# Kernel tuning notes

Measured on AMD Instinct MI355X. Metric: run time of the kernel, lower is better.

The kernel has to match this reference:

```python
import jax, jax.numpy as jnp
import numpy as np

HEADS = 4


def setup_inputs() -> dict:
    key = jax.random.key(0)
    ks = jax.random.split(key, 6)
    b, c, d, h, w = 4, 512, 16, 16, 16
    x = jax.random.normal(ks[0], (b, c, d, h, w), dtype=jnp.float32)
    s = 0.02  # param init scale
    Wq = jax.random.normal(ks[1], (c, c), dtype=jnp.float32) * s
    Wk = jax.random.normal(ks[2], (c, c), dtype=jnp.float32) * s
    Wv = jax.random.normal(ks[3], (c, c), dtype=jnp.float32) * s
    Wproj = jax.random.normal(ks[4], (c, c), dtype=jnp.float32) * s
    bproj = jnp.zeros((c,), dtype=jnp.float32)
    return {"x": x, "Wq": Wq, "Wk": Wk, "Wv": Wv, "Wproj": Wproj, "bproj": bproj}


def reference(x, Wq, Wk, Wv, Wproj, bproj):
    b, c, d, h, w = x.shape
    N = d * h * w
    scale = (c // HEADS) ** -0.5  # module uses ch//heads for scale
    xf = x.reshape(b, c, N)  # (b, c, N)
    # 1x1 Conv1d == channel matmul
    q = jnp.einsum('oc,bcn->bon', Wq, xf)
    k = jnp.einsum('oc,bcn->bon', Wk, xf)
    v = jnp.einsum('oc,bcn->bon', Wv, xf)
    # Faithful to original (buggy) view: split SEQUENCE dim by heads -> (b, H, c, N//H)
    q = q.reshape(b, HEADS, c, N // HEADS)
    k = k.reshape(b, HEADS, c, N // HEADS)
    v = v.reshape(b, HEADS, c, N // HEADS)
    attn = jax.nn.softmax(jnp.einsum('bhqe,bhke->bhqk', q, k) * scale, axis=-1)
    out = jnp.einsum('bhqk,bhke->bhqe', attn, v)  # (b, H, c, N//H)
    out = jnp.swapaxes(out, 2, 3).reshape(b, c, N)  # matches transpose(2,3).view
    out = jnp.einsum('oc,bcn->bon', Wproj, out) + bproj[None, :, None]
    return out.reshape(b, c, d, h, w) + x
```

## Files before the change

kernel.cpp:

```cpp
#include <hip/hip_runtime.h>
#include <stdint.h>


typedef __attribute__((ext_vector_type(8))) short short8;
typedef __attribute__((ext_vector_type(4))) float f32x4;

typedef const __attribute__((address_space(1))) unsigned int* gas_ptr;
typedef __attribute__((address_space(3))) unsigned int* las_ptr;

#define ATTN_SCALE 0.08838834764831845f

__device__ __forceinline__ unsigned short f2bf(float f) {
    union { float f; unsigned int u; } c; c.f = f;
    unsigned int u = c.u;
    u += 0x7fffu + ((u >> 16) & 1u);
    return (unsigned short)(u >> 16);
}

__device__ __forceinline__ void gl_lds16(const void* g, void* l) {
    __builtin_amdgcn_global_load_lds((gas_ptr)(uintptr_t)g, (las_ptr)(uintptr_t)l,
                                     16, 0, 0);
}

template<int LDA, int LDB, int KDIM, bool PERMB = false>
__device__ __forceinline__ void mfma_core(
    const unsigned short* __restrict__ A,
    const unsigned short* __restrict__ B,
    int m0, int n0,
    unsigned short* __restrict__ sA, unsigned short* __restrict__ sB,
    f32x4 acc[4][4])
{
    const int tid  = threadIdx.x;
    const int lane = tid & 63, wave = tid >> 6;
    const int lr = lane >> 2, lc = lane & 3;
    const int lcs = lc ^ ((lr >> 1) & 3);
    const int wm = (wave & 1) * 64, wn = (wave >> 1) * 64;
    const int col = lane & 15, quad = lane >> 4;
    const int swz = (quad ^ ((col >> 1) & 3)) * 8;

    const unsigned short* ga = A + (size_t)(m0 + 32 * wave + lr) * LDA + lcs * 8;
    int rb0 = n0 + 32 * wave + lr;
    int rb1 = rb0 + 16;
    if (PERMB) {
        rb0 = 4 * (rb0 & 127) + (rb0 >> 7);
        rb1 = 4 * (rb1 & 127) + (rb1 >> 7);
    }
    const unsigned short* gb0 = B + (size_t)rb0 * LDB + lcs * 8;
    const unsigned short* gb1 = B + (size_t)rb1 * LDB + lcs * 8;

    const int wr0 = (32 * wave) * 32;
    const int wr1 = (32 * wave + 16) * 32;

    gl_lds16(ga,            sA + wr0);
    gl_lds16(ga + 16 * LDA, sA + wr1);
    gl_lds16(gb0,           sB + wr0);
    gl_lds16(gb1,           sB + wr1);

    constexpr int NK = KDIM / 32;
    for (int kk = 0; kk < NK; ++kk) {
        const int bo = (kk & 1) * 4096;
        if (kk + 1 < NK) {
            const int nb = ((kk + 1) & 1) * 4096;
            const int k0 = (kk + 1) * 32;
            gl_lds16(ga + k0,            sA + nb + wr0);
            gl_lds16(ga + k0 + 16 * LDA, sA + nb + wr1);
            gl_lds16(gb0 + k0,           sB + nb + wr0);
            gl_lds16(gb1 + k0,           sB + nb + wr1);
            asm volatile("s_waitcnt vmcnt(4)" ::: "memory");
        } else {
            asm volatile("s_waitcnt vmcnt(0)" ::: "memory");
        }
        __builtin_amdgcn_s_barrier();
        asm volatile("" ::: "memory");
        __builtin_amdgcn_sched_barrier(0);

        const unsigned short* bA = sA + bo;
        const unsigned short* bB = sB + bo;
        short8 af[4], bfv[4];
        #pragma unroll
        for (int i = 0; i < 4; ++i)
            af[i] = *(const short8*)&bA[(wm + i * 16 + col) * 32 + swz];
        #pragma unroll
        for (int j = 0; j < 4; ++j)
            bfv[j] = *(const short8*)&bB[(wn + j * 16 + col) * 32 + swz];
        #pragma unroll
        for (int i = 0; i < 4; ++i)
            #pragma unroll
            for (int j = 0; j < 4; ++j)
                acc[i][j] = __builtin_amdgcn_mfma_f32_16x16x32_bf16(
                    af[i], bfv[j], acc[i][j], 0, 0, 0);

        __builtin_amdgcn_s_barrier();
        asm volatile("" ::: "memory");
    }
}

__global__ __launch_bounds__(256)
void prep(const float* __restrict__ x,
          const float* __restrict__ Wq, const float* __restrict__ Wk,
          const float* __restrict__ Wv, const float* __restrict__ Wp,
          unsigned short* __restrict__ xT, unsigned short* __restrict__ Wb)
{
    if (blockIdx.z == 4) {
        const int idx = (blockIdx.y * 64 + blockIdx.x) * 256 + threadIdx.x;
        const int mat = idx >> 16;
        const int off = (idx & 65535) << 2;
        const float* src = (mat == 0 ? Wq : mat == 1 ? Wk : mat == 2 ? Wv : Wp) + off;
        const float4 f = *(const float4*)src;
        uint2 o;
        o.x = f2bf(f.x) | ((unsigned)f2bf(f.y) << 16);
        o.y = f2bf(f.z) | ((unsigned)f2bf(f.w) << 16);
        *(uint2*)&Wb[mat * 262144 + off] = o;
        return;
    }
    const int b = blockIdx.z;
    const int l = threadIdx.x & 63, w = threadIdx.x >> 6;
    const int n  = blockIdx.x * 64 + l;
    const int c0 = blockIdx.y * 32 + w * 8;
    const float* xp = x + (size_t)b * 2097152 + (size_t)c0 * 4096 + n;
    unsigned int p[4];
    #pragma unroll
    for (int j = 0; j < 4; ++j) {
        const unsigned short a  = f2bf(xp[(2 * j)     * 4096]);
        const unsigned short bb = f2bf(xp[(2 * j + 1) * 4096]);
        p[j] = a | ((unsigned)bb << 16);
    }
    uint4 v; v.x = p[0]; v.y = p[1]; v.z = p[2]; v.w = p[3];
    *(uint4*)&xT[(size_t)b * 2097152 + (size_t)n * 512 + c0] = v;
}

__global__ __launch_bounds__(256)
void gemm_qkv(const unsigned short* __restrict__ Wb,
              const unsigned short* __restrict__ xT,
              unsigned short* __restrict__ qb, unsigned short* __restrict__ kb,
              unsigned short* __restrict__ vT)
{
    __shared__ unsigned short sA[2 * 128 * 32], sB[2 * 128 * 32];

    const int z = blockIdx.z, wsel = z >> 2, b = z & 3;
    const unsigned short* A = Wb + wsel * 262144;
    const unsigned short* B = xT + (size_t)b * 2097152;
    const int m0 = blockIdx.y * 128, n0 = blockIdx.x * 128;

    f32x4 z4 = {0.f, 0.f, 0.f, 0.f};
    f32x4 acc[4][4];
    #pragma unroll
    for (int i = 0; i < 4; ++i)
        #pragma unroll
        for (int j = 0; j < 4; ++j) acc[i][j] = z4;

    mfma_core<512, 512, 512>(A, B, m0, n0, sA, sB, acc);

    const int lane = threadIdx.x & 63, wave = threadIdx.x >> 6;
    const int wm = (wave & 1) * 64, wn = (wave >> 1) * 64;
    const int col = lane & 15, quad = lane >> 4;

    if (wsel < 2) {
        unsigned short* C = (wsel == 0 ? qb : kb) + (size_t)b * 2097152;
        #pragma unroll
        for (int i = 0; i < 4; ++i)
            #pragma unroll
            for (int r = 0; r < 4; ++r) {
                const int row = m0 + wm + i * 16 + quad * 4 + r;
                #pragma unroll
                for (int j = 0; j < 4; ++j)
                    C[(size_t)row * 4096 + n0 + wn + j * 16 + col] = f2bf(acc[i][j][r]);
            }
    } else {
        const int h = m0 >> 7, s = n0 >> 10, e0 = n0 & 1023;
        unsigned short* dst = vT + (size_t)(b * 4 + h) * 524288 + s * 128;
        #pragma unroll
        for (int i = 0; i < 4; ++i) {
            const int kb2 = wm + i * 16 + quad * 4;
            #pragma unroll
            for (int j = 0; j < 4; ++j) {
                const int e = e0 + wn + j * 16 + col;
                uint2 o;
                o.x = f2bf(acc[i][j][0]) | ((unsigned)f2bf(acc[i][j][1]) << 16);
                o.y = f2bf(acc[i][j][2]) | ((unsigned)f2bf(acc[i][j][3]) << 16);
                *(uint2*)&dst[(size_t)e * 512 + kb2] = o;
            }
        }
    }
}

__global__ __launch_bounds__(256)
void gemm_qks(const unsigned short* __restrict__ qb,
              const unsigned short* __restrict__ kb,
              unsigned short* __restrict__ P)
{
    __shared__ float red[2][32][4];
    const int d = blockIdx.x + 16 * blockIdx.y;
    const int flat = (d & 7) * 32 + (d >> 3);
    const int rg = flat & 15, z = flat >> 4;
    const unsigned short* Aq = qb + (size_t)z * 524288;
    const unsigned short* Bk = kb + (size_t)z * 524288;
    unsigned short* Pz = P + (size_t)z * 262144;

    const int lane = threadIdx.x & 63, w = threadIdx.x >> 6;
    const int col = lane & 15, quad = lane >> 4;

    const unsigned short* a0 = Aq + (size_t)(rg * 32 + col) * 1024 + quad * 8;
    const unsigned short* a1 = a0 + 16 * 1024;
    const unsigned short* bp[8];
    #pragma unroll
    for (int g = 0; g < 8; ++g) {
        const int n = w * 128 + g * 16 + col;
        const int r = 4 * (n & 127) + (n >> 7);
        bp[g] = Bk + (size_t)r * 1024 + quad * 8;
    }

    f32x4 z4 = {0.f, 0.f, 0.f, 0.f};
    f32x4 acc[2][8];
    #pragma unroll
    for (int f = 0; f < 2; ++f)
        #pragma unroll
        for (int g = 0; g < 8; ++g) acc[f][g] = z4;

    #pragma unroll 2
    for (int k0 = 0; k0 < 1024; k0 += 32) {
        const short8 af0 = *(const short8*)(a0 + k0);
        const short8 af1 = *(const short8*)(a1 + k0);
        short8 bf[8];
        #pragma unroll
        for (int g = 0; g < 8; ++g) bf[g] = *(const short8*)(bp[g] + k0);
        #pragma unroll
        for (int g = 0; g < 8; ++g)
            acc[0][g] = __builtin_amdgcn_mfma_f32_16x16x32_bf16(
                af0, bf[g], acc[0][g], 0, 0, 0);
        #pragma unroll
        for (int g = 0; g < 8; ++g)
            acc[1][g] = __builtin_amdgcn_mfma_f32_16x16x32_bf16(
                af1, bf[g], acc[1][g], 0, 0, 0);
    }

    float mx[2][4];
    #pragma unroll
    for (int f = 0; f < 2; ++f)
        #pragma unroll
        for (int r = 0; r < 4; ++r) {
            float m = acc[f][0][r];
            #pragma unroll
            for (int g = 1; g < 8; ++g) m = fmaxf(m, acc[f][g][r]);
            #pragma unroll
            for (int s = 1; s < 16; s <<= 1) m = fmaxf(m, __shfl_xor(m, s));
            mx[f][r] = m;
        }
    if (col == 0) {
        #pragma unroll
        for (int f = 0; f < 2; ++f)
            #pragma unroll
            for (int r = 0; r < 4; ++r)
                red[0][f * 16 + quad * 4 + r][w] = mx[f][r];
    }
    __syncthreads();
    float sm[2][4];
    #pragma unroll
    for (int f = 0; f < 2; ++f)
        #pragma unroll
        for (int r = 0; r < 4; ++r) {
            const int row = f * 16 + quad * 4 + r;
            const float m = fmaxf(fmaxf(red[0][row][0], red[0][row][1]),
                                  fmaxf(red[0][row][2], red[0][row][3]));
            float s = 0.f;
            #pragma unroll
            for (int g = 0; g < 8; ++g) {
                const float e = __expf((acc[f][g][r] - m) * ATTN_SCALE);
                acc[f][g][r] = e;
                s += e;
            }
            #pragma unroll
            for (int t = 1; t < 16; t <<= 1) s += __shfl_xor(s, t);
            sm[f][r] = s;
        }
    if (col == 0) {
        #pragma unroll
        for (int f = 0; f < 2; ++f)
            #pragma unroll
            for (int r = 0; r < 4; ++r)
                red[1][f * 16 + quad * 4 + r][w] = sm[f][r];
    }
    __syncthreads();
    #pragma unroll
    for (int f = 0; f < 2; ++f)
        #pragma unroll
        for (int r = 0; r < 4; ++r) {
            const int row = f * 16 + quad * 4 + r;
            const float tot = red[1][row][0] + red[1][row][1]
                            + red[1][row][2] + red[1][row][3];
            const float inv = 1.f / tot;
            unsigned short* op = Pz + (size_t)(rg * 32 + row) * 512
                               + w * 128 + col;
            #pragma unroll
            for (int g = 0; g < 8; ++g)
                op[g * 16] = f2bf(acc[f][g][r] * inv);
        }
}

__global__ __launch_bounds__(256)
void gemm_pv(const unsigned short* __restrict__ Pb,
             const unsigned short* __restrict__ vT,
             unsigned short* __restrict__ yT)
{
    __shared__ unsigned short sT[128 * 136];
    unsigned short* sA = sT;
    unsigned short* sB = sT + 8192;
    const int z = blockIdx.z, b = z >> 2, hh = z & 3;
    const unsigned short* A = Pb + (size_t)z * 262144;
    const unsigned short* B = vT + (size_t)z * 524288;
    unsigned short* yTb = yT + (size_t)b * 2097152;
    const int m0 = blockIdx.y * 128;
    const int n0 = blockIdx.x * 128;

    f32x4 z4 = {0.f, 0.f, 0.f, 0.f};
    f32x4 acc[4][4];
    #pragma unroll
    for (int i = 0; i < 4; ++i)
        #pragma unroll
        for (int j = 0; j < 4; ++j) acc[i][j] = z4;

    mfma_core<512, 512, 512>(A, B, m0, n0, sA, sB, acc);

    __syncthreads();

    const int tid = threadIdx.x;
    const int lane = tid & 63, wave = tid >> 6;
    const int wm = (wave & 1) * 64, wn = (wave >> 1) * 64;
    const int col = lane & 15, quad = lane >> 4;

    #pragma unroll
    for (int i = 0; i < 4; ++i)
        #pragma unroll
        for (int r = 0; r < 4; ++r) {
            const int rr = wm + i * 16 + quad * 4 + r;
            #pragma unroll
            for (int j = 0; j < 4; ++j)
                sT[rr * 136 + wn + j * 16 + col] = f2bf(acc[i][j][r]);
        }
    __syncthreads();

    #pragma unroll
    for (int k = 0; k < 4; ++k) {
        const int rid = k * 256 + tid;
        const int qq_l = rid >> 3, s = rid & 7;
        const unsigned short* Trow = sT + qq_l * 136;
        unsigned int p[8];
        #pragma unroll
        for (int t = 0; t < 8; ++t) {
            const unsigned int a  = Trow[s + 8 * (2 * t)];
            const unsigned int bb = Trow[s + 8 * (2 * t + 1)];
            p[t] = a | (bb << 16);
        }
        const size_t base = (size_t)((s << 9) + m0 + qq_l) * 512 + hh * 128 + (n0 >> 3);
        uint4 lo; lo.x = p[0]; lo.y = p[1]; lo.z = p[2]; lo.w = p[3];
        uint4 hi; hi.x = p[4]; hi.y = p[5]; hi.z = p[6]; hi.w = p[7];
        *(uint4*)&yTb[base]     = lo;
        *(uint4*)&yTb[base + 8] = hi;
    }
}

__global__ __launch_bounds__(256)
void gemm_proj(const unsigned short* __restrict__ Wpb,
               const unsigned short* __restrict__ yT,
               const float* __restrict__ bias, const float* __restrict__ x,
               float* __restrict__ out)
{
    __shared__ unsigned short sA[2 * 128 * 32], sB[2 * 128 * 32];
    const int b = blockIdx.z;
    const unsigned short* B = yT + (size_t)b * 2097152;
    const int m0 = blockIdx.y * 128, n0 = blockIdx.x * 128;

    f32x4 z4 = {0.f, 0.f, 0.f, 0.f};
    f32x4 acc[4][4];
    #pragma unroll
    for (int i = 0; i < 4; ++i)
        #pragma unroll
        for (int j = 0; j < 4; ++j) acc[i][j] = z4;

    mfma_core<512, 512, 512>(Wpb, B, m0, n0, sA, sB, acc);

    const int lane = threadIdx.x & 63, wave = threadIdx.x >> 6;
    const int wm = (wave & 1) * 64, wn = (wave >> 1) * 64;
    const int col = lane & 15, quad = lane >> 4;
    const size_t boff = (size_t)b * 2097152;
    #pragma unroll
    for (int i = 0; i < 4; ++i)
        #pragma unroll
        for (int r = 0; r < 4; ++r) {
            const int row = m0 + wm + i * 16 + quad * 4 + r;
            const float bi = bias[row];
            #pragma unroll
            for (int j = 0; j < 4; ++j) {
                const size_t idx = boff + (size_t)row * 4096 + n0 + wn + j * 16 + col;
                out[idx] = acc[i][j][r] + bi + x[idx];
            }
        }
}

extern "C" void kernel_launch(void* const* d_in, const int* in_sizes, int n_in,
                              void* d_out, int out_size, void* d_ws, size_t ws_size,
                              hipStream_t stream) {
    const float* x     = (const float*)d_in[0];
    const float* Wq    = (const float*)d_in[1];
    const float* Wk    = (const float*)d_in[2];
    const float* Wv    = (const float*)d_in[3];
    const float* Wproj = (const float*)d_in[4];
    const float* bproj = (const float*)d_in[5];
    float* out = (float*)d_out;

    char* w = (char*)d_ws;
    unsigned short* xT = (unsigned short*)(w + 0);
    unsigned short* qb = (unsigned short*)(w + 16777216);
    unsigned short* kb = (unsigned short*)(w + 33554432);
    unsigned short* vT = (unsigned short*)(w + 50331648);
    unsigned short* Pb = (unsigned short*)(w + 100663296);
    unsigned short* Wb = (unsigned short*)(w + 109051904);
    unsigned short* yT = xT;

    prep        <<<dim3(64, 16, 5),  256, 0, stream>>>(x, Wq, Wk, Wv, Wproj, xT, Wb);
    gemm_qkv    <<<dim3(32, 4, 12),  256, 0, stream>>>(Wb, xT, qb, kb, vT);
    gemm_qks    <<<dim3(16, 16),     256, 0, stream>>>(qb, kb, Pb);
    gemm_pv     <<<dim3(8, 4, 16),   256, 0, stream>>>(Pb, vT, yT);
    gemm_proj   <<<dim3(32, 4, 4),   256, 0, stream>>>(Wb + 3 * 262144, yT, bproj, x, out);
}
```

Before: 215.8 us.

## Store Q/K in MFMA-fragment-packed layout and use 8-wave QK softmax blocks

Result: faster. 191.0 us (-11.5%).

```diff
diff --git a/kernel.cpp b/kernel.cpp
--- a/kernel.cpp
+++ b/kernel.cpp
@@ -156,16 +156,28 @@
     const int col = lane & 15, quad = lane >> 4;
 
     if (wsel < 2) {
-        unsigned short* C = (wsel == 0 ? qb : kb) + (size_t)b * 2097152;
-        #pragma unroll
-        for (int i = 0; i < 4; ++i)
-            #pragma unroll
-            for (int r = 0; r < 4; ++r) {
-                const int row = m0 + wm + i * 16 + quad * 4 + r;
+        unsigned short* C = (wsel == 0 ? qb : kb)
+                          + (size_t)(b * 4 + (m0 >> 7)) * 524288;
+        const int s  = n0 >> 10;
+        const int e0 = (n0 & 1023) + wn;
+        const int tq = wm + quad * 4;
+        #pragma unroll
+        for (int i = 0; i < 4; ++i) {
+            #pragma unroll
+            for (int j = 0; j < 4; ++j) {
+                const int e  = e0 + j * 16 + col;
+                const int Kc = e >> 5, qc = (e >> 3) & 3, el = e & 7;
                 #pragma unroll
-                for (int j = 0; j < 4; ++j)
-                    C[(size_t)row * 4096 + n0 + wn + j * 16 + col] = f2bf(acc[i][j][r]);
+                for (int r = 0; r < 4; ++r) {
+                    const int t = tq + i * 16 + r;
+                    int R, cc;
+                    if (wsel == 0) { R = t >> 2;           cc = 4 * (t & 3) + s; }
+                    else           { R = s * 8 + (t >> 4); cc = t & 15; }
+                    C[(R * 32 + Kc) * 512 + (qc * 16 + cc) * 8 + el] =
+                        f2bf(acc[i][j][r]);
+                }
             }
+        }
     } else {
         const int h = m0 >> 7, s = n0 >> 10, e0 = n0 & 1023;
         unsigned short* dst = vT + (size_t)(b * 4 + h) * 524288 + s * 128;
@@ -184,52 +196,53 @@
     }
 }
 
-__global__ __launch_bounds__(256)
+__global__ __launch_bounds__(512)
 void gemm_qks(const unsigned short* __restrict__ qb,
               const unsigned short* __restrict__ kb,
               unsigned short* __restrict__ P)
 {
-    __shared__ float red[2][32][4];
-    const int d = blockIdx.x + 16 * blockIdx.y;
+    __shared__ float red[2][32][8];
+    const int d = blockIdx.x;
     const int flat = (d & 7) * 32 + (d >> 3);
     const int rg = flat & 15, z = flat >> 4;
     const unsigned short* Aq = qb + (size_t)z * 524288;
     const unsigned short* Bk = kb + (size_t)z * 524288;
     unsigned short* Pz = P + (size_t)z * 262144;
 
-    const int lane = threadIdx.x & 63, w = threadIdx.x >> 6;
+    const int tid = threadIdx.x;
+    const int lane = tid & 63, w = tid >> 6;
     const int col = lane & 15, quad = lane >> 4;
 
-    const unsigned short* a0 = Aq + (size_t)(rg * 32 + col) * 1024 + quad * 8;
-    const unsigned short* a1 = a0 + 16 * 1024;
-    const unsigned short* bp[8];
-    #pragma unroll
-    for (int g = 0; g < 8; ++g) {
-        const int n = w * 128 + g * 16 + col;
-        const int r = 4 * (n & 127) + (n >> 7);
-        bp[g] = Bk + (size_t)r * 1024 + quad * 8;
-    }
+    const unsigned short* ap0 = Aq + (size_t)((rg * 2 + 0) * 32) * 512 + lane * 8;
+    const unsigned short* ap1 = Aq + (size_t)((rg * 2 + 1) * 32) * 512 + lane * 8;
+    const unsigned short* bp0 = Bk + (size_t)((w * 4 + 0) * 32) * 512 + lane * 8;
+    const unsigned short* bp1 = bp0 + 16384;
+    const unsigned short* bp2 = bp0 + 32768;
+    const unsigned short* bp3 = bp0 + 49152;
 
     f32x4 z4 = {0.f, 0.f, 0.f, 0.f};
-    f32x4 acc[2][8];
+    f32x4 acc[2][4];
     #pragma unroll
     for (int f = 0; f < 2; ++f)
         #pragma unroll
-        for (int g = 0; g < 8; ++g) acc[f][g] = z4;
-
-    #pragma unroll 2
-    for (int k0 = 0; k0 < 1024; k0 += 32) {
-        const short8 af0 = *(const short8*)(a0 + k0);
-        const short8 af1 = *(const short8*)(a1 + k0);
-        short8 bf[8];
-        #pragma unroll
-        for (int g = 0; g < 8; ++g) bf[g] = *(const short8*)(bp[g] + k0);
-        #pragma unroll
-        for (int g = 0; g < 8; ++g)
+        for (int g = 0; g < 4; ++g) acc[f][g] = z4;
+
+    #pragma unroll 4
+    for (int kk = 0; kk < 32; ++kk) {
+        const int o = kk * 512;
+        const short8 af0 = *(const short8*)(ap0 + o);
+        const short8 af1 = *(const short8*)(ap1 + o);
+        short8 bf[4];
+        bf[0] = *(const short8*)(bp0 + o);
+        bf[1] = *(const short8*)(bp1 + o);
+        bf[2] = *(const short8*)(bp2 + o);
+        bf[3] = *(const short8*)(bp3 + o);
+        #pragma unroll
+        for (int g = 0; g < 4; ++g)
             acc[0][g] = __builtin_amdgcn_mfma_f32_16x16x32_bf16(
                 af0, bf[g], acc[0][g], 0, 0, 0);
         #pragma unroll
-        for (int g = 0; g < 8; ++g)
+        for (int g = 0; g < 4; ++g)
             acc[1][g] = __builtin_amdgcn_mfma_f32_16x16x32_bf16(
                 af1, bf[g], acc[1][g], 0, 0, 0);
     }
@@ -241,7 +254,7 @@
         for (int r = 0; r < 4; ++r) {
             float m = acc[f][0][r];
             #pragma unroll
-            for (int g = 1; g < 8; ++g) m = fmaxf(m, acc[f][g][r]);
+            for (int g = 1; g < 4; ++g) m = fmaxf(m, acc[f][g][r]);
             #pragma unroll
             for (int s = 1; s < 16; s <<= 1) m = fmaxf(m, __shfl_xor(m, s));
             mx[f][r] = m;
@@ -260,11 +273,12 @@
         #pragma unroll
         for (int r = 0; r < 4; ++r) {
             const int row = f * 16 + quad * 4 + r;
-            const float m = fmaxf(fmaxf(red[0][row][0], red[0][row][1]),
-                                  fmaxf(red[0][row][2], red[0][row][3]));
+            float m = red[0][row][0];
+            #pragma unroll
+            for (int t = 1; t < 8; ++t) m = fmaxf(m, red[0][row][t]);
             float s = 0.f;
             #pragma unroll
-            for (int g = 0; g < 8; ++g) {
+            for (int g = 0; g < 4; ++g) {
                 const float e = __expf((acc[f][g][r] - m) * ATTN_SCALE);
                 acc[f][g][r] = e;
                 s += e;
@@ -286,13 +300,14 @@
         #pragma unroll
         for (int r = 0; r < 4; ++r) {
             const int row = f * 16 + quad * 4 + r;
-            const float tot = red[1][row][0] + red[1][row][1]
-                            + red[1][row][2] + red[1][row][3];
+            float tot = red[1][row][0];
+            #pragma unroll
+            for (int t = 1; t < 8; ++t) tot += red[1][row][t];
             const float inv = 1.f / tot;
             unsigned short* op = Pz + (size_t)(rg * 32 + row) * 512
-                               + w * 128 + col;
-            #pragma unroll
-            for (int g = 0; g < 8; ++g)
+                               + w * 64 + col;
+            #pragma unroll
+            for (int g = 0; g < 4; ++g)
                 op[g * 16] = f2bf(acc[f][g][r] * inv);
         }
 }
@@ -419,7 +434,7 @@
 
     prep        <<<dim3(64, 16, 5),  256, 0, stream>>>(x, Wq, Wk, Wv, Wproj, xT, Wb);
     gemm_qkv    <<<dim3(32, 4, 12),  256, 0, stream>>>(Wb, xT, qb, kb, vT);
-    gemm_qks    <<<dim3(16, 16),     256, 0, stream>>>(qb, kb, Pb);
+    gemm_qks    <<<dim3(256),        512, 0, stream>>>(qb, kb, Pb);
     gemm_pv     <<<dim3(8, 4, 16),   256, 0, stream>>>(Pb, vT, yT);
     gemm_proj   <<<dim3(32, 4, 4),   256, 0, stream>>>(Wb + 3 * 262144, yT, bproj, x, out);
 }
```
